# Kernel tuning notes

Hardware: AMD Instinct MI355X
Metric: run time of the kernel (lower is better)

## Reference

```python
import jax, jax.numpy as jnp
import numpy as np
from math import pi

K_MAX = 0.1   # init k
DLT_K = 0.02  # init dk
EPS = 0.1

N_IMG, N_ATOM = 32, 400000


def _dot(a, b):
    # sum over last two dims, keepdims -> shape [..., 1, 1]
    return jnp.sum(a * b, axis=(-2, -1), keepdims=True)


def _norm(a):
    return jnp.sqrt(_dot(a, a))


def setup_inputs() -> dict:
    key = jax.random.key(0)
    k1, k2, k3 = jax.random.split(key, 3)
    pos = jax.random.normal(k1, (N_IMG, N_ATOM, 3), dtype=jnp.float32)
    frc = jax.random.normal(k2, (N_IMG, N_ATOM, 3), dtype=jnp.float32)
    eng = jax.random.normal(k3, (N_IMG,), dtype=jnp.float32)
    # ensure climbing-image argmax lies in the interior (valid frc_para index)
    eng = eng.at[N_IMG // 2].add(10.0)
    return {"pos": pos, "frc": frc, "eng": eng}


def reference(pos, frc, eng):
    dtype = pos.dtype
    eng3 = eng[:, None, None]  # [N,1,1]

    # ---- spring force k per segment: [N-1,1,1] ----
    eng_ref = jnp.min(eng3) - EPS
    eng_max = jnp.max(eng3)
    eng_i = jnp.maximum(eng3[1:], eng3[:-1])
    k = K_MAX - DLT_K * (eng_max - eng_i) / (eng_max - eng_ref)
    k = jnp.where(eng_i < eng_ref, K_MAX - DLT_K, k)

    # ---- improved tangent estimation: [N-2, A, 3] ----
    tau_p = pos[1:-1] - pos[:-2]
    tau_m = pos[2:] - pos[1:-1]
    e0, e1, e2 = eng3[:-2], eng3[1:-1], eng3[2:]
    msk_pp = ((e2 > e1) & (e1 > e0)).astype(dtype)
    msk_mm = ((e2 < e1) & (e1 < e0)).astype(dtype)
    not_both = 1.0 - jnp.maximum(msk_pp, msk_mm)
    msk_p = (e2 > e1).astype(dtype) * not_both
    msk_m = (e2 < e1).astype(dtype) * not_both
    dv_max = jnp.maximum(jnp.abs(e2 - e1), jnp.abs(e0 - e1))
    dv_min = jnp.minimum(jnp.abs(e2 - e1), jnp.abs(e0 - e1))
    tau = (tau_p * msk_pp + tau_m * msk_mm
           + (tau_p * dv_max + tau_m * dv_min) * msk_p
           + (tau_p * dv_min + tau_m * dv_max) * msk_m)
    tau = tau / _norm(tau)

    # ---- NEB force decomposition ----
    frc_in = frc[1:-1]
    vecp = pos[2:] - pos[1:-1]
    vecm = pos[1:-1] - pos[:-2]
    frc_para = _dot(frc_in, tau) * tau
    spr = k[1:] * vecp - k[:-1] * vecm
    spr_para = (k[1:] * _norm(vecp) - k[:-1] * _norm(vecm)) * tau
    frc_perp = frc_in - frc_para  # uses pre-climbing frc_para (torch in-place order)
    spr_perp = spr - spr_para

    # climbing image: double parallel force at the highest-energy image
    i = jnp.argmax(eng) - 1  # eng index -> frc_para index offset (interior images)
    # torch indexes frc_para with the raw eng argmax; reproduce that indexing
    i_raw = jnp.argmax(eng)
    frc_para = frc_para.at[i_raw].multiply(2.0)

    frc_neb = spr_para - frc_para  # nudged=True

    # doubly nudged switch term
    sw = (2.0 / pi) * jnp.arctan2(_dot(frc_perp, frc_perp), _dot(spr_perp, spr_perp))
    doubly = spr_perp - _dot(spr_perp, frc_perp) * frc_perp * sw
    frc_neb = frc_neb + doubly

    out_frc = frc + jnp.pad(frc_neb, ((1, 1), (0, 0), (0, 0)))
    return out_frc
```

## Files before the change

kernel.cpp:

```cpp
#include <hip/hip_runtime.h>
#include <math.h>

#define N_IMG 32
#define N_ATOM 400000
#define NE (N_ATOM*3)
#define NE4 (NE/4)
#define KMAXC 0.1f
#define DLTKC 0.02f
#define EPSE 0.1f

#define OFF_SDD 0
#define OFF_SPM 31
#define OFF_SFP 61
#define OFF_SFM 91
#define OFF_SFF 121
#define NSUM 151
#define OFF_CO 160

__device__ __forceinline__ float dot4(float4 a, float4 b) {
    return a.x*b.x + a.y*b.y + a.z*b.z + a.w*b.w;
}
__device__ __forceinline__ float4 sub4(float4 a, float4 b) {
    return make_float4(a.x-b.x, a.y-b.y, a.z-b.z, a.w-b.w);
}
__device__ __forceinline__ float wred64(float v) {
#pragma unroll
    for (int m = 32; m >= 1; m >>= 1) v += __shfl_xor(v, m, 64);
    return v;
}

__global__ __launch_bounds__(256) void eb_pass1(const float* __restrict__ pos,
                                                const float* __restrict__ frc,
                                                float* __restrict__ sums) {
    __shared__ float ls[NSUM];
    for (int i = threadIdx.x; i < NSUM; i += 256) ls[i] = 0.f;
    __syncthreads();

    const int t = blockIdx.x * 256 + threadIdx.x;
    const bool act = t < NE4;
    const float4* pos4 = reinterpret_cast<const float4*>(pos);
    const float4* frc4 = reinterpret_cast<const float4*>(frc);
    const float4 z4 = make_float4(0.f, 0.f, 0.f, 0.f);
    const int lane = threadIdx.x & 63;

    float4 p_prev = act ? pos4[t] : z4;
    float4 d_prev = z4;
#pragma unroll 1
    for (int r = 1; r < N_IMG; ++r) {
        float4 p = act ? pos4[(size_t)r * NE4 + t] : z4;
        float4 d = sub4(p, p_prev);
        float sdd = wred64(dot4(d, d));
        if (lane == 0) atomicAdd(&ls[OFF_SDD + (r - 1)], sdd);
        if (r >= 2) {
            float4 f = act ? frc4[(size_t)(r - 1) * NE4 + t] : z4;
            float spm = wred64(dot4(d_prev, d));
            float sfp = wred64(dot4(f, d_prev));
            float sfm = wred64(dot4(f, d));
            float sff = wred64(dot4(f, f));
            if (lane == 0) {
                int jj = r - 2;
                atomicAdd(&ls[OFF_SPM + jj], spm);
                atomicAdd(&ls[OFF_SFP + jj], sfp);
                atomicAdd(&ls[OFF_SFM + jj], sfm);
                atomicAdd(&ls[OFF_SFF + jj], sff);
            }
        }
        p_prev = p;
        d_prev = d;
    }
    __syncthreads();
    for (int i = threadIdx.x; i < NSUM; i += 256) atomicAdd(&sums[i], ls[i]);
}

__global__ void eb_coeff(const float* __restrict__ eng,
                         const float* __restrict__ sums,
                         float* __restrict__ co) {
    if (threadIdx.x != 0 || blockIdx.x != 0) return;
    float e[N_IMG];
    float emin = 1e30f, emax = -1e30f;
    int imax = 0;
    for (int i = 0; i < N_IMG; ++i) {
        float v = eng[i];
        e[i] = v;
        if (v < emin) emin = v;
        if (v > emax) { emax = v; imax = i; }
    }
    const float eref = emin - EPSE;
    float k[N_IMG - 1];
    for (int l = 0; l < N_IMG - 1; ++l) {
        float ei = fmaxf(e[l + 1], e[l]);
        float kk = KMAXC - DLTKC * (emax - ei) / (emax - eref);
        if (ei < eref) kk = KMAXC - DLTKC;
        k[l] = kk;
    }
    for (int jj = 0; jj < N_IMG - 2; ++jj) {
        float e0 = e[jj], e1 = e[jj + 1], e2 = e[jj + 2];
        float km = k[jj], kp = k[jj + 1];
        float pp = (e2 > e1 && e1 > e0) ? 1.f : 0.f;
        float mm = (e2 < e1 && e1 < e0) ? 1.f : 0.f;
        float nb = 1.f - fmaxf(pp, mm);
        float mp = ((e2 > e1) ? 1.f : 0.f) * nb;
        float mq = ((e2 < e1) ? 1.f : 0.f) * nb;
        float dvmax = fmaxf(fabsf(e2 - e1), fabsf(e0 - e1));
        float dvmin = fminf(fabsf(e2 - e1), fabsf(e0 - e1));
        float a = pp + dvmax * mp + dvmin * mq;
        float b = mm + dvmin * mp + dvmax * mq;
        float Spp = sums[OFF_SDD + jj];
        float Smm = sums[OFF_SDD + jj + 1];
        float Spm = sums[OFF_SPM + jj];
        float Sfp = sums[OFF_SFP + jj];
        float Sfm = sums[OFF_SFM + jj];
        float Sff = sums[OFF_SFF + jj];
        float ntau2 = a * a * Spp + 2.f * a * b * Spm + b * b * Smm;
        float ntau = sqrtf(ntau2);
        float ta = a / ntau, tb = b / ntau;
        float fpar = ta * Sfp + tb * Sfm;
        float spar = kp * sqrtf(Smm) - km * sqrtf(Spp);
        float ffpp = Sff - fpar * fpar;
        float strau = ta * (kp * Spm - km * Spp) + tb * (kp * Smm - km * Spm);
        float Sss = kp * kp * Smm - 2.f * kp * km * Spm + km * km * Spp;
        float sspp = Sss - 2.f * spar * strau + spar * spar;
        float Ssf = kp * Sfm - km * Sfp;
        float spfp = Ssf - fpar * strau;
        float sw = (2.0f / 3.14159265358979323846f) * atan2f(ffpp, sspp);
        float c = spfp * sw;
        float g = (jj == imax) ? 2.f : 1.f;
        float w = (c - g) * fpar / ntau;
        co[jj]      = 1.f - c;
        co[30 + jj] = kp + w * b;
        co[60 + jj] = w * a - km;
    }
}

__global__ __launch_bounds__(256) void eb_pass2(const float* __restrict__ pos,
                                                const float* __restrict__ frc,
                                                const float* __restrict__ co,
                                                float* __restrict__ out) {
    __shared__ float A[30], B[30], C[30];
    if (threadIdx.x < 30) {
        A[threadIdx.x] = co[threadIdx.x];
        B[threadIdx.x] = co[30 + threadIdx.x];
        C[threadIdx.x] = co[60 + threadIdx.x];
    }
    __syncthreads();
    const int t = blockIdx.x * 256 + threadIdx.x;
    if (t >= NE4) return;
    const float4* pos4 = reinterpret_cast<const float4*>(pos);
    const float4* frc4 = reinterpret_cast<const float4*>(frc);
    float4* out4 = reinterpret_cast<float4*>(out);

    size_t i31 = (size_t)31 * NE4 + t;
    float4 p_next = pos4[i31];
    out4[i31] = frc4[i31];
    float4 p30 = pos4[(size_t)30 * NE4 + t];
    float4 d_next = sub4(p_next, p30);
    p_next = p30;
#pragma unroll 1
    for (int l = 29; l >= 0; --l) {
        float4 p = pos4[(size_t)l * NE4 + t];
        float4 d = sub4(p_next, p);
        float4 f = frc4[(size_t)(l + 1) * NE4 + t];
        float ca = A[l], cb = B[l], cc = C[l];
        float4 o;
        o.x = ca * f.x + cb * d_next.x + cc * d.x;
        o.y = ca * f.y + cb * d_next.y + cc * d.y;
        o.z = ca * f.z + cb * d_next.z + cc * d.z;
        o.w = ca * f.w + cb * d_next.w + cc * d.w;
        out4[(size_t)(l + 1) * NE4 + t] = o;
        d_next = d;
        p_next = p;
    }
    out4[t] = frc4[t];
}

extern "C" void kernel_launch(void* const* d_in, const int* in_sizes, int n_in,
                              void* d_out, int out_size, void* d_ws, size_t ws_size,
                              hipStream_t stream) {
    const float* pos = (const float*)d_in[0];
    const float* frc = (const float*)d_in[1];
    const float* eng = (const float*)d_in[2];
    float* out = (float*)d_out;
    float* ws = (float*)d_ws;

    hipMemsetAsync(d_ws, 0, NSUM * sizeof(float), stream);
    const int blocks = (NE4 + 255) / 256;
    eb_pass1<<<blocks, 256, 0, stream>>>(pos, frc, ws);
    eb_coeff<<<1, 64, 0, stream>>>(eng, ws, ws + OFF_CO);
    eb_pass2<<<blocks, 256, 0, stream>>>(pos, frc, ws + OFF_CO, out);
}
```

Baseline: 453.4 us.

## Use DPP wave reductions, unroll image loops, parallelize coefficient kernel

Replaces the shuffle-based 64-lane reductions in the first pass with DPP row-shift and row-broadcast adds, so the total ends in lane 63. The loop is restructured to peel the first image, which removes the per-iteration branch. Both passes now unroll their image loops by 5 so more loads can be in flight. The coefficient kernel runs one thread per segment instead of a single serial thread. These cut reduction latency and per-iteration overhead in a memory-bound streaming pass, at the cost of more registers.

```diff
diff --git a/kernel.cpp b/kernel.cpp
--- a/kernel.cpp
+++ b/kernel.cpp
@@ -23,10 +23,15 @@
 __device__ __forceinline__ float4 sub4(float4 a, float4 b) {
     return make_float4(a.x-b.x, a.y-b.y, a.z-b.z, a.w-b.w);
 }
-__device__ __forceinline__ float wred64(float v) {
-#pragma unroll
-    for (int m = 32; m >= 1; m >>= 1) v += __shfl_xor(v, m, 64);
-    return v;
+
+__device__ __forceinline__ float wred_dpp(float x) {
+    x += __int_as_float(__builtin_amdgcn_update_dpp(0, __float_as_int(x), 0x111, 0xf, 0xf, false));
+    x += __int_as_float(__builtin_amdgcn_update_dpp(0, __float_as_int(x), 0x112, 0xf, 0xf, false));
+    x += __int_as_float(__builtin_amdgcn_update_dpp(0, __float_as_int(x), 0x114, 0xf, 0xf, false));
+    x += __int_as_float(__builtin_amdgcn_update_dpp(0, __float_as_int(x), 0x118, 0xf, 0xf, false));
+    x += __int_as_float(__builtin_amdgcn_update_dpp(0, __float_as_int(x), 0x142, 0xa, 0xf, false));
+    x += __int_as_float(__builtin_amdgcn_update_dpp(0, __float_as_int(x), 0x143, 0xc, 0xf, false));
+    return x;
 }
 
 __global__ __launch_bounds__(256) void eb_pass1(const float* __restrict__ pos,
@@ -43,27 +48,32 @@
     const float4 z4 = make_float4(0.f, 0.f, 0.f, 0.f);
     const int lane = threadIdx.x & 63;
 
-    float4 p_prev = act ? pos4[t] : z4;
-    float4 d_prev = z4;
-#pragma unroll 1
-    for (int r = 1; r < N_IMG; ++r) {
+    float4 p0 = act ? pos4[t] : z4;
+    float4 p1 = act ? pos4[(size_t)NE4 + t] : z4;
+    float4 d_prev = sub4(p1, p0);
+    {
+        float sdd = wred_dpp(dot4(d_prev, d_prev));
+        if (lane == 63) atomicAdd(&ls[OFF_SDD + 0], sdd);
+    }
+    float4 p_prev = p1;
+
+#pragma unroll 5
+    for (int r = 2; r < N_IMG; ++r) {
         float4 p = act ? pos4[(size_t)r * NE4 + t] : z4;
+        float4 f = act ? frc4[(size_t)(r - 1) * NE4 + t] : z4;
         float4 d = sub4(p, p_prev);
-        float sdd = wred64(dot4(d, d));
-        if (lane == 0) atomicAdd(&ls[OFF_SDD + (r - 1)], sdd);
-        if (r >= 2) {
-            float4 f = act ? frc4[(size_t)(r - 1) * NE4 + t] : z4;
-            float spm = wred64(dot4(d_prev, d));
-            float sfp = wred64(dot4(f, d_prev));
-            float sfm = wred64(dot4(f, d));
-            float sff = wred64(dot4(f, f));
-            if (lane == 0) {
-                int jj = r - 2;
-                atomicAdd(&ls[OFF_SPM + jj], spm);
-                atomicAdd(&ls[OFF_SFP + jj], sfp);
-                atomicAdd(&ls[OFF_SFM + jj], sfm);
-                atomicAdd(&ls[OFF_SFF + jj], sff);
-            }
+        float sdd = wred_dpp(dot4(d, d));
+        float spm = wred_dpp(dot4(d_prev, d));
+        float sfp = wred_dpp(dot4(f, d_prev));
+        float sfm = wred_dpp(dot4(f, d));
+        float sff = wred_dpp(dot4(f, f));
+        if (lane == 63) {
+            int jj = r - 2;
+            atomicAdd(&ls[OFF_SDD + (r - 1)], sdd);
+            atomicAdd(&ls[OFF_SPM + jj], spm);
+            atomicAdd(&ls[OFF_SFP + jj], sfp);
+            atomicAdd(&ls[OFF_SFM + jj], sfm);
+            atomicAdd(&ls[OFF_SFF + jj], sff);
         }
         p_prev = p;
         d_prev = d;
@@ -75,7 +85,8 @@
 __global__ void eb_coeff(const float* __restrict__ eng,
                          const float* __restrict__ sums,
                          float* __restrict__ co) {
-    if (threadIdx.x != 0 || blockIdx.x != 0) return;
+    const int jj = threadIdx.x;
+    if (jj >= N_IMG - 2 || blockIdx.x != 0) return;
     float e[N_IMG];
     float emin = 1e30f, emax = -1e30f;
     int imax = 0;
@@ -86,50 +97,47 @@
         if (v > emax) { emax = v; imax = i; }
     }
     const float eref = emin - EPSE;
-    float k[N_IMG - 1];
-    for (int l = 0; l < N_IMG - 1; ++l) {
-        float ei = fmaxf(e[l + 1], e[l]);
-        float kk = KMAXC - DLTKC * (emax - ei) / (emax - eref);
-        if (ei < eref) kk = KMAXC - DLTKC;
-        k[l] = kk;
-    }
-    for (int jj = 0; jj < N_IMG - 2; ++jj) {
-        float e0 = e[jj], e1 = e[jj + 1], e2 = e[jj + 2];
-        float km = k[jj], kp = k[jj + 1];
-        float pp = (e2 > e1 && e1 > e0) ? 1.f : 0.f;
-        float mm = (e2 < e1 && e1 < e0) ? 1.f : 0.f;
-        float nb = 1.f - fmaxf(pp, mm);
-        float mp = ((e2 > e1) ? 1.f : 0.f) * nb;
-        float mq = ((e2 < e1) ? 1.f : 0.f) * nb;
-        float dvmax = fmaxf(fabsf(e2 - e1), fabsf(e0 - e1));
-        float dvmin = fminf(fabsf(e2 - e1), fabsf(e0 - e1));
-        float a = pp + dvmax * mp + dvmin * mq;
-        float b = mm + dvmin * mp + dvmax * mq;
-        float Spp = sums[OFF_SDD + jj];
-        float Smm = sums[OFF_SDD + jj + 1];
-        float Spm = sums[OFF_SPM + jj];
-        float Sfp = sums[OFF_SFP + jj];
-        float Sfm = sums[OFF_SFM + jj];
-        float Sff = sums[OFF_SFF + jj];
-        float ntau2 = a * a * Spp + 2.f * a * b * Spm + b * b * Smm;
-        float ntau = sqrtf(ntau2);
-        float ta = a / ntau, tb = b / ntau;
-        float fpar = ta * Sfp + tb * Sfm;
-        float spar = kp * sqrtf(Smm) - km * sqrtf(Spp);
-        float ffpp = Sff - fpar * fpar;
-        float strau = ta * (kp * Spm - km * Spp) + tb * (kp * Smm - km * Spm);
-        float Sss = kp * kp * Smm - 2.f * kp * km * Spm + km * km * Spp;
-        float sspp = Sss - 2.f * spar * strau + spar * spar;
-        float Ssf = kp * Sfm - km * Sfp;
-        float spfp = Ssf - fpar * strau;
-        float sw = (2.0f / 3.14159265358979323846f) * atan2f(ffpp, sspp);
-        float c = spfp * sw;
-        float g = (jj == imax) ? 2.f : 1.f;
-        float w = (c - g) * fpar / ntau;
-        co[jj]      = 1.f - c;
-        co[30 + jj] = kp + w * b;
-        co[60 + jj] = w * a - km;
-    }
+    float e0 = e[jj], e1 = e[jj + 1], e2 = e[jj + 2];
+    float eim = fmaxf(e1, e0);
+    float km = KMAXC - DLTKC * (emax - eim) / (emax - eref);
+    if (eim < eref) km = KMAXC - DLTKC;
+    float eip = fmaxf(e2, e1);
+    float kp = KMAXC - DLTKC * (emax - eip) / (emax - eref);
+    if (eip < eref) kp = KMAXC - DLTKC;
+
+    float pp = (e2 > e1 && e1 > e0) ? 1.f : 0.f;
+    float mm = (e2 < e1 && e1 < e0) ? 1.f : 0.f;
+    float nb = 1.f - fmaxf(pp, mm);
+    float mp = ((e2 > e1) ? 1.f : 0.f) * nb;
+    float mq = ((e2 < e1) ? 1.f : 0.f) * nb;
+    float dvmax = fmaxf(fabsf(e2 - e1), fabsf(e0 - e1));
+    float dvmin = fminf(fabsf(e2 - e1), fabsf(e0 - e1));
+    float a = pp + dvmax * mp + dvmin * mq;
+    float b = mm + dvmin * mp + dvmax * mq;
+    float Spp = sums[OFF_SDD + jj];
+    float Smm = sums[OFF_SDD + jj + 1];
+    float Spm = sums[OFF_SPM + jj];
+    float Sfp = sums[OFF_SFP + jj];
+    float Sfm = sums[OFF_SFM + jj];
+    float Sff = sums[OFF_SFF + jj];
+    float ntau2 = a * a * Spp + 2.f * a * b * Spm + b * b * Smm;
+    float ntau = sqrtf(ntau2);
+    float ta = a / ntau, tb = b / ntau;
+    float fpar = ta * Sfp + tb * Sfm;
+    float spar = kp * sqrtf(Smm) - km * sqrtf(Spp);
+    float ffpp = Sff - fpar * fpar;
+    float strau = ta * (kp * Spm - km * Spp) + tb * (kp * Smm - km * Spm);
+    float Sss = kp * kp * Smm - 2.f * kp * km * Spm + km * km * Spp;
+    float sspp = Sss - 2.f * spar * strau + spar * spar;
+    float Ssf = kp * Sfm - km * Sfp;
+    float spfp = Ssf - fpar * strau;
+    float sw = (2.0f / 3.14159265358979323846f) * atan2f(ffpp, sspp);
+    float c = spfp * sw;
+    float g = (jj == imax) ? 2.f : 1.f;
+    float w = (c - g) * fpar / ntau;
+    co[jj]      = 1.f - c;
+    co[30 + jj] = kp + w * b;
+    co[60 + jj] = w * a - km;
 }
 
 __global__ __launch_bounds__(256) void eb_pass2(const float* __restrict__ pos,
@@ -155,7 +163,7 @@
     float4 p30 = pos4[(size_t)30 * NE4 + t];
     float4 d_next = sub4(p_next, p30);
     p_next = p30;
-#pragma unroll 1
+#pragma unroll 5
     for (int l = 29; l >= 0; --l) {
         float4 p = pos4[(size_t)l * NE4 + t];
         float4 d = sub4(p_next, p);
```

Result: faster. 440.3 us (-2.9%).
